# Optimization experiments

Hardware: AMD Instinct MI355X
Metric: run time of the kernel (lower is better)

## Reference

```python
import jax, jax.numpy as jnp
import numpy as np

CODEBOOK_SIZE = 8192
EMBED_DIM = 128
BETA = 0.25
TEMPERATURE = 0.1
EPS_NORM = 1e-12  # torch F.normalize eps


def _l2_normalize(x, axis=-1):
    n = jnp.linalg.norm(x, axis=axis, keepdims=True)
    return x / jnp.maximum(n, EPS_NORM)


def setup_inputs() -> dict:
    key = jax.random.key(0)
    kz, kw = jax.random.split(key)
    z = jax.random.normal(kz, (4, 4096, EMBED_DIM), dtype=jnp.float32)
    # torch init is uniform(-1/D, 1/D); normal also exercises the math fine,
    # but stay faithful to scale:
    W = jax.random.uniform(kw, (CODEBOOK_SIZE, EMBED_DIM), dtype=jnp.float32,
                           minval=-1.0 / EMBED_DIM, maxval=1.0 / EMBED_DIM)
    return {"z": z, "W": W}


def reference(z, W):
    orig_shape = z.shape
    z_flat = z.reshape(-1, EMBED_DIM)              # [N, D]
    N = z_flat.shape[0]

    z_norm = _l2_normalize(z_flat, axis=1)
    e_norm = _l2_normalize(W, axis=1)
    scores = z_norm @ e_norm.T                     # [N, K]

    idx = jnp.argmax(scores, axis=1)               # [N]
    z_q = W[idx].reshape(orig_shape)

    counts = jnp.zeros((CODEBOOK_SIZE,), jnp.float32).at[idx].add(1.0)
    e_mean = counts / N
    perplexity = jnp.exp(-jnp.sum(e_mean * jnp.log(e_mean + 1e-8)))

    sg = jax.lax.stop_gradient
    commit_loss = jnp.mean((sg(z_q) - z) ** 2) + BETA * jnp.mean((z_q - sg(z)) ** 2)

    z_q_st = z + sg(z_q - z)                        # straight-through

    log_probs = jax.nn.log_softmax(scores / TEMPERATURE, axis=1)  # [N, K]
    probs = jnp.exp(log_probs)
    P_avg = jnp.mean(probs, axis=0) + 1e-8
    entropy_loss = -jnp.sum(P_avg * jnp.log(P_avg))

    return (z_q_st, commit_loss, perplexity, entropy_loss)
```

## Files before the change

kernel.cpp:

```cpp
#include <hip/hip_runtime.h>
#include <hip/hip_bf16.h>
#include <math.h>

#define N_ROWS 16384
#define DIM 128
#define K_CODES 8192
#define EPS2 2e-3f
#define EPSF 7e-5f

#define OFF_EN       0u
#define OFF_ZN       1048576u
#define OFF_EP       3145728u
#define OFF_ZP       4194304u
#define OFF_ZC       6291456u
#define OFF_PART     7340032u
#define OFF_PART2    7602176u
#define OFF_LINV     7864320u
#define OFF_IDX      7880704u
#define OFF_FLA      7897088u
#define OFF_FLB      7913472u
#define OFF_CNT      7929856u
#define OFF_P        7938048u
#define OFF_MSE      7946240u
#define OFF_NFA      7946241u
#define OFF_NFB      7946242u
#define OFF_REFBUF   7946244u
#define MEMSET_BYTES 196624u

typedef __bf16 bf16x8 __attribute__((ext_vector_type(8)));
typedef float  f32x4  __attribute__((ext_vector_type(4)));
#define MFMA16(a, b, c) __builtin_amdgcn_mfma_f32_16x16x32_bf16(a, b, c, 0, 0, 0)

__device__ __forceinline__ void gld_lds16(const ushort* g, ushort* l) {
    __builtin_amdgcn_global_load_lds(
        (const __attribute__((address_space(1))) unsigned int*)g,
        (__attribute__((address_space(3))) unsigned int*)l, 16, 0, 0);
}

__device__ __forceinline__ ushort f2bf(float x) {
    __hip_bfloat16 b = __float2bfloat16(x);
    return *reinterpret_cast<ushort*>(&b);
}
__device__ __forceinline__ float bf2f(ushort u) {
    __hip_bfloat16 b = *reinterpret_cast<__hip_bfloat16*>(&u);
    return __bfloat162float(b);
}

__device__ __forceinline__ void bf_store2(ushort* __restrict__ P, int T, int r,
                                          int rx, int k, ushort e0, ushort e1) {
    int g = k >> 6, kp = (k >> 3) & 7, j = k & 7;
    int off = (((((T << 2) + g) << 10) + (r << 3) + (kp ^ rx)) << 3) + j;
    *reinterpret_cast<ushort2*>(&P[off]) = make_ushort2(e0, e1);
}

__global__ __launch_bounds__(256) void k_prep(const float* __restrict__ z,
                                              const float* __restrict__ W,
                                              float* __restrict__ zN,
                                              float* __restrict__ eN,
                                              ushort* __restrict__ Zp,
                                              ushort* __restrict__ Ep) {
    int t = threadIdx.x, w = t >> 6, lane = t & 63;
    int row = blockIdx.x * 4 + w;
    const float* src; float* dstN; ushort* dstP;
    if (row < N_ROWS) { src = z; dstN = zN; dstP = Zp; }
    else { row -= N_ROWS; src = W; dstN = eN; dstP = Ep; }
    float2 v = *reinterpret_cast<const float2*>(&src[(size_t)row * DIM + lane * 2]);
    float ss = v.x * v.x + v.y * v.y;
#pragma unroll
    for (int off = 32; off; off >>= 1) ss += __shfl_xor(ss, off);
    float nrm = fmaxf(sqrtf(ss), 1e-12f);
    float a = v.x / nrm, b = v.y / nrm;
    *reinterpret_cast<float2*>(&dstN[(size_t)row * DIM + lane * 2]) = make_float2(a, b);
    ushort ha = f2bf(a), hb = f2bf(b);
    ushort la = f2bf(a - bf2f(ha)), lb = f2bf(b - bf2f(hb));
    int T = row >> 7, r = row & 127, rx = r & 7, d = lane * 2;
    bf_store2(dstP, T, r, rx, d, ha, hb);
    bf_store2(dstP, T, r, rx, 128 + d, la, lb);
}

__global__ __launch_bounds__(256, 2) void k_p1(const ushort* __restrict__ Zp,
                                               const ushort* __restrict__ Ep,
                                               float4* __restrict__ part) {
    __shared__ ushort Bu[2][16384];
    int t = threadIdx.x, lane = t & 63, w = t >> 6;
    int rg = blockIdx.x >> 2, slice = blockIdx.x & 3;
    int wm = w >> 1, wn = w & 1;
    int n15 = lane & 15, quad = lane >> 4;
    int T = rg >> 1, rofs = (rg & 1) << 6;

    bf16x8 af[2][2][2];
#pragma unroll
    for (int ms = 0; ms < 2; ++ms) {
        int r = rofs + wm * 32 + ms * 16 + n15, rx = r & 7;
#pragma unroll
        for (int g = 0; g < 2; ++g)
#pragma unroll
            for (int kl = 0; kl < 2; ++kl)
                af[ms][g][kl] = *reinterpret_cast<const bf16x8*>(
                    &Zp[(((((T << 2) + g) << 10) + (r << 3) + (((kl * 4 + quad)) ^ rx)) << 3)]);
    }

    float sm[8], s2v[8], sl[8];
    unsigned si[8];
#pragma unroll
    for (int s = 0; s < 8; ++s) { sm[s] = -1e30f; s2v[s] = -1e30f; sl[s] = 0.f; si[s] = 0u; }

    {
        const ushort* gb = Ep + (((size_t)(slice * 16) << 2) << 13);
#pragma unroll
        for (int it = 0; it < 8; ++it) {
            int cpos = it * 256 + t;
            gld_lds16(gb + (cpos << 3), &Bu[0][cpos << 3]);
        }
    }
    int bufc = 0;
    for (int ch = 0; ch < 16; ++ch) {
        __syncthreads();
        if (ch < 15) {
            const ushort* gb = Ep + (((size_t)((slice * 16 + ch + 1) << 2)) << 13);
            ushort* dst = Bu[bufc ^ 1];
#pragma unroll
            for (int it = 0; it < 8; ++it) {
                int cpos = it * 256 + t;
                gld_lds16(gb + (cpos << 3), &dst[cpos << 3]);
            }
        }
        const ushort* bsrc = Bu[bufc];
        f32x4 acc[2][4];
#pragma unroll
        for (int i = 0; i < 2; ++i)
#pragma unroll
            for (int j = 0; j < 4; ++j) acc[i][j] = (f32x4)2.0f;
#pragma unroll
        for (int g = 0; g < 2; ++g)
#pragma unroll
            for (int kl = 0; kl < 2; ++kl) {
                bf16x8 bfr[4];
#pragma unroll
                for (int ns = 0; ns < 4; ++ns) {
                    int c = wn * 64 + ns * 16 + n15;
                    int kx = (kl * 4 + quad) ^ (c & 7);
                    bfr[ns] = *reinterpret_cast<const bf16x8*>(
                        &bsrc[(((g << 10) + (c << 3) + kx) << 3)]);
                }
#pragma unroll
                for (int ms = 0; ms < 2; ++ms)
#pragma unroll
                    for (int ns = 0; ns < 4; ++ns)
                        acc[ms][ns] = MFMA16(af[ms][g][kl], bfr[ns], acc[ms][ns]);
            }
        unsigned cbase = (unsigned)((slice * 16 + ch) * 128 + wn * 64 + n15);
#pragma unroll
        for (int ms = 0; ms < 2; ++ms)
#pragma unroll
            for (int reg = 0; reg < 4; ++reg) {
                int s = ms * 4 + reg;
                float m = sm[s], m2 = s2v[s], l = 0.f;
                unsigned idx = si[s];
#pragma unroll
                for (int ns = 0; ns < 4; ++ns) {
                    float v = acc[ms][ns][reg];
                    l += __expf(fmaf(v, 10.f, -20.f));
                    float lo = fminf(v, m);
                    m2 = fmaxf(m2, lo);
                    idx = (v > m) ? (cbase + ns * 16) : idx;
                    m = fmaxf(v, m);
                }
                sl[s] += l; sm[s] = m; s2v[s] = m2; si[s] = idx;
            }
        bufc ^= 1;
    }
#pragma unroll
    for (int ms = 0; ms < 2; ++ms)
#pragma unroll
        for (int reg = 0; reg < 4; ++reg) {
            int s = ms * 4 + reg;
            float m = sm[s], m2 = s2v[s], l = sl[s];
            unsigned idx = si[s];
#pragma unroll
            for (int off = 1; off < 16; off <<= 1) {
                float om  = __shfl_xor(m, off);
                float om2 = __shfl_xor(m2, off);
                float ol  = __shfl_xor(l, off);
                unsigned oi = (unsigned)__shfl_xor((int)idx, off);
                m2 = fmaxf(fmaxf(m2, om2), fminf(m, om));
                l += ol;
                bool take = (om > m) || (om == m && oi < idx);
                idx = take ? oi : idx;
                m = fmaxf(m, om);
            }
            if (n15 == 0) {
                int row = rg * 64 + wm * 32 + ms * 16 + quad * 4 + reg;
                part[slice * N_ROWS + row] = make_float4(m, l, __uint_as_float(idx), m2);
            }
        }
}

__global__ __launch_bounds__(256) void k_merge(const float4* __restrict__ part,
                                               float* __restrict__ linv_out,
                                               int* __restrict__ idx_out,
                                               unsigned int* __restrict__ counts,
                                               int* __restrict__ flaglistA,
                                               int* __restrict__ nfA) {
    int row = blockIdx.x * 256 + threadIdx.x;
    float m = -1e30f, m2 = -1e30f, l = 0.f;
    unsigned idx = 0u;
#pragma unroll
    for (int s = 0; s < 4; ++s) {
        float4 p = part[s * N_ROWS + row];
        float om = p.x, ol = p.y, om2 = p.w;
        unsigned oi = __float_as_uint(p.z);
        m2 = fmaxf(fmaxf(m2, om2), fminf(m, om));
        l += ol;
        bool take = (om > m) || (om == m && oi < idx);
        idx = take ? oi : idx;
        m = fmaxf(m, om);
    }
    linv_out[row] = 1.0f / l;
    idx_out[row] = (int)idx;
    atomicAdd(&counts[idx], 1u);
    if (m - m2 < EPS2) {
        int pos = atomicAdd(nfA, 1);
        if (pos < 8192) flaglistA[pos] = row;
    }
}

__global__ __launch_bounds__(256) void k_gather2(const ushort* __restrict__ Zp,
                                                 const int* __restrict__ flaglistA,
                                                 const int* __restrict__ nfA,
                                                 ushort* __restrict__ Zc) {
    int nf2 = *nfA; if (nf2 > 8192) nf2 = 8192;
    int total = nf2 * 32;
    const uint4* srcv = reinterpret_cast<const uint4*>(Zp);
    uint4* dstv = reinterpret_cast<uint4*>(Zc);
    for (int c = blockIdx.x * 256 + threadIdx.x; c < total; c += 65536) {
        int crow = c >> 5, g = (c >> 3) & 3, kp = c & 7;
        int row = flaglistA[crow];
        int Ts = row >> 7, rs = row & 127;
        int sidx = (((Ts << 2) + g) << 10) + (rs << 3) + (kp ^ (rs & 7));
        int Td = crow >> 6, rd = crow & 63;
        int didx = (((Td << 2) + g) << 9) + (rd << 3) + (kp ^ (rd & 7));
        dstv[didx] = srcv[sidx];
    }
}

__global__ __launch_bounds__(256, 2) void k_s2(const ushort* __restrict__ Zc,
                                               const ushort* __restrict__ Ep,
                                               const int* __restrict__ nfA,
                                               float4* __restrict__ part2) {
    __shared__ ushort Bu[2][8192];
    int nf2 = *nfA; if (nf2 > 8192) nf2 = 8192;
    int cg2 = blockIdx.x >> 3, csl = blockIdx.x & 7;
    if (cg2 * 64 >= nf2) return;
    int t = threadIdx.x, lane = t & 63, w = t >> 6;
    int wm = w >> 1, wn = w & 1;
    int n15 = lane & 15, quad = lane >> 4;

    bf16x8 af[2][4][2];
#pragma unroll
    for (int ms = 0; ms < 2; ++ms) {
        int r = wm * 32 + ms * 16 + n15, rx = r & 7;
#pragma unroll
        for (int gz = 0; gz < 4; ++gz)
#pragma unroll
            for (int kl = 0; kl < 2; ++kl)
                af[ms][gz][kl] = *reinterpret_cast<const bf16x8*>(
                    &Zc[(((((cg2 << 2) + gz) << 9) + (r << 3) + ((kl * 4 + quad) ^ rx)) << 3)]);
    }

    float sm[8], s2v[8];
    unsigned si[8];
#pragma unroll
    for (int s = 0; s < 8; ++s) { sm[s] = -1e30f; s2v[s] = -1e30f; si[s] = 0u; }

    {
        const ushort* gb = Ep + (((size_t)((csl * 8) << 2)) << 13);
#pragma unroll
        for (int it = 0; it < 4; ++it) {
            int cpos = it * 256 + t;
            gld_lds16(gb + (cpos << 3), &Bu[0][cpos << 3]);
        }
    }
    int bufc = 0;
    f32x4 acc[2][4];
#pragma unroll
    for (int i = 0; i < 2; ++i)
#pragma unroll
        for (int j = 0; j < 4; ++j) acc[i][j] = (f32x4)2.0f;

    for (int st = 0; st < 32; ++st) {
        __syncthreads();
        if (st < 31) {
            int nx = st + 1;
            const ushort* gb = Ep + (((size_t)(((csl * 8 + (nx >> 2)) << 2) + (nx & 3))) << 13);
            ushort* dst = Bu[bufc ^ 1];
#pragma unroll
            for (int it = 0; it < 4; ++it) {
                int cpos = it * 256 + t;
                gld_lds16(gb + (cpos << 3), &dst[cpos << 3]);
            }
        }
        const ushort* bsrc = Bu[bufc];
        int ge = st & 3;
        int a0 = ge & 1, a1 = (ge & 1) + 2;
        bool two = (ge < 2);
#pragma unroll
        for (int kl = 0; kl < 2; ++kl) {
            bf16x8 bfr[4];
#pragma unroll
            for (int ns = 0; ns < 4; ++ns) {
                int c = wn * 64 + ns * 16 + n15;
                int kx = (kl * 4 + quad) ^ (c & 7);
                bfr[ns] = *reinterpret_cast<const bf16x8*>(&bsrc[(((c << 3) + kx) << 3)]);
            }
#pragma unroll
            for (int ms = 0; ms < 2; ++ms)
#pragma unroll
                for (int ns = 0; ns < 4; ++ns)
                    acc[ms][ns] = MFMA16(af[ms][a0][kl], bfr[ns], acc[ms][ns]);
            if (two) {
#pragma unroll
                for (int ms = 0; ms < 2; ++ms)
#pragma unroll
                    for (int ns = 0; ns < 4; ++ns)
                        acc[ms][ns] = MFMA16(af[ms][a1][kl], bfr[ns], acc[ms][ns]);
            }
        }
        if (ge == 3) {
            int ch = st >> 2;
            unsigned cbase = (unsigned)((csl * 8 + ch) * 128 + wn * 64 + n15);
#pragma unroll
            for (int ms = 0; ms < 2; ++ms)
#pragma unroll
                for (int reg = 0; reg < 4; ++reg) {
                    int s = ms * 4 + reg;
                    float m = sm[s], m2 = s2v[s];
                    unsigned idx = si[s];
#pragma unroll
                    for (int ns = 0; ns < 4; ++ns) {
                        float v = acc[ms][ns][reg];
                        float lo = fminf(v, m);
                        m2 = fmaxf(m2, lo);
                        idx = (v > m) ? (cbase + ns * 16) : idx;
                        m = fmaxf(v, m);
                    }
                    sm[s] = m; s2v[s] = m2; si[s] = idx;
                }
#pragma unroll
            for (int i = 0; i < 2; ++i)
#pragma unroll
                for (int j = 0; j < 4; ++j) acc[i][j] = (f32x4)2.0f;
        }
        bufc ^= 1;
    }
#pragma unroll
    for (int ms = 0; ms < 2; ++ms)
#pragma unroll
        for (int reg = 0; reg < 4; ++reg) {
            int s = ms * 4 + reg;
            float m = sm[s], m2 = s2v[s];
            unsigned idx = si[s];
#pragma unroll
            for (int off = 1; off < 16; off <<= 1) {
                float om  = __shfl_xor(m, off);
                float om2 = __shfl_xor(m2, off);
                unsigned oi = (unsigned)__shfl_xor((int)idx, off);
                m2 = fmaxf(fmaxf(m2, om2), fminf(m, om));
                bool take = (om > m) || (om == m && oi < idx);
                idx = take ? oi : idx;
                m = fmaxf(m, om);
            }
            if (n15 == 0) {
                int crow = cg2 * 64 + wm * 32 + ms * 16 + quad * 4 + reg;
                part2[csl * 8192 + crow] = make_float4(m, 0.f, __uint_as_float(idx), m2);
            }
        }
}

__global__ __launch_bounds__(256) void k_merge2(const float4* __restrict__ part2,
                                                const int* __restrict__ flaglistA,
                                                const int* __restrict__ nfA,
                                                int* __restrict__ idx_arr,
                                                unsigned int* __restrict__ counts,
                                                int* __restrict__ flaglistB,
                                                int* __restrict__ nfB) {
    int i = blockIdx.x * 256 + threadIdx.x;
    int nf2 = *nfA; if (nf2 > 8192) nf2 = 8192;
    if (i >= nf2) return;
    int row = flaglistA[i];
    float m = -1e30f, m2 = -1e30f;
    unsigned idx = 0u;
#pragma unroll
    for (int s = 0; s < 8; ++s) {
        float4 p = part2[s * 8192 + i];
        float om = p.x, om2 = p.w;
        unsigned oi = __float_as_uint(p.z);
        m2 = fmaxf(fmaxf(m2, om2), fminf(m, om));
        bool take = (om > m) || (om == m && oi < idx);
        idx = take ? oi : idx;
        m = fmaxf(m, om);
    }
    int newi = (int)idx, oldi = idx_arr[row];
    if (newi != oldi) {
        idx_arr[row] = newi;
        atomicAdd(&counts[oldi], 0xFFFFFFFFu);
        atomicAdd(&counts[newi], 1u);
    }
    if (m - m2 < EPSF) {
        int pos = atomicAdd(nfB, 1);
        if (pos < N_ROWS) flaglistB[pos] = row;
    }
}

__global__ __launch_bounds__(256) void k_refine(const float* __restrict__ zN,
                                                const float* __restrict__ eN,
                                                const int* __restrict__ flaglistB,
                                                const int* __restrict__ nfB,
                                                unsigned long long* __restrict__ refbuf) {
    int nf = *nfB;
    if (nf > N_ROWS) nf = N_ROWS;
    int csl = blockIdx.x & 7;
    int t = threadIdx.x;
    __shared__ float zl[DIM];
    for (int fi = blockIdx.x >> 3; fi < nf; fi += 512) {
        int row = flaglistB[fi];
        __syncthreads();
        if (t < DIM) zl[t] = zN[(size_t)row * DIM + t];
        __syncthreads();
        double best = -1e300;
        int bc = 0x7FFFFFFF;
#pragma unroll
        for (int j = 0; j < 4; ++j) {
            int c = csl * 1024 + j * 256 + t;
            const float* e = &eN[(size_t)c * DIM];
            double s = 0.0;
#pragma unroll 8
            for (int d = 0; d < DIM; ++d) s += (double)zl[d] * (double)e[d];
            if (s > best) { best = s; bc = c; }
        }
#pragma unroll
        for (int off = 1; off < 64; off <<= 1) {
            double ob = __shfl_xor(best, off);
            int oc = __shfl_xor(bc, off);
            if (ob > best || (ob == best && oc < bc)) { best = ob; bc = oc; }
        }
        if ((t & 63) == 0) {
            unsigned long long u = (unsigned long long)__double_as_longlong(best);
            u = (u & 0x8000000000000000ull) ? ~u : (u | 0x8000000000000000ull);
            unsigned long long key = (u & ~0x1FFFull) | (unsigned long long)(8191 - bc);
            atomicMax(&refbuf[row], key);
        }
    }
}

__global__ __launch_bounds__(256) void k_fixidx(const int* __restrict__ flaglistB,
                                                const int* __restrict__ nfB,
                                                const unsigned long long* __restrict__ refbuf,
                                                int* __restrict__ idx,
                                                unsigned int* __restrict__ counts) {
    int i = blockIdx.x * 256 + threadIdx.x;
    int nf = *nfB;
    if (nf > N_ROWS) nf = N_ROWS;
    if (i < nf) {
        int row = flaglistB[i];
        int newi = 8191 - (int)(refbuf[row] & 0x1FFFull);
        int oldi = idx[row];
        if (newi != oldi) {
            idx[row] = newi;
            atomicAdd(&counts[oldi], 0xFFFFFFFFu);
            atomicAdd(&counts[newi], 1u);
        }
    }
}

__global__ __launch_bounds__(256, 2) void k_p2(const ushort* __restrict__ Zp,
                                               const ushort* __restrict__ Ep,
                                               const float* __restrict__ linv_in,
                                               float* __restrict__ P_sum) {
    __shared__ ushort Bu[2][16384];
    int t = threadIdx.x, lane = t & 63, w = t >> 6;
    int cg = blockIdx.x >> 2, rslice = blockIdx.x & 3;
    int wm = w >> 1, wn = w & 1;
    int n15 = lane & 15, quad = lane >> 4;
    int T = cg >> 1, cofs = (cg & 1) << 6;

    bf16x8 af[2][2][2];
#pragma unroll
    for (int ms = 0; ms < 2; ++ms) {
        int c = cofs + wm * 32 + ms * 16 + n15, cx = c & 7;
#pragma unroll
        for (int g = 0; g < 2; ++g)
#pragma unroll
            for (int kl = 0; kl < 2; ++kl)
                af[ms][g][kl] = *reinterpret_cast<const bf16x8*>(
                    &Ep[(((((T << 2) + g) << 10) + (c << 3) + ((kl * 4 + quad) ^ cx)) << 3)]);
    }

    float pacc[8];
#pragma unroll
    for (int s = 0; s < 8; ++s) pacc[s] = 0.f;

    {
        const ushort* gb = Zp + (((size_t)((rslice * 32) << 2)) << 13);
#pragma unroll
        for (int it = 0; it < 8; ++it) {
            int cpos = it * 256 + t;
            gld_lds16(gb + (cpos << 3), &Bu[0][cpos << 3]);
        }
    }
    int bufc = 0;
    for (int ch = 0; ch < 32; ++ch) {
        __syncthreads();
        if (ch < 31) {
            const ushort* gb = Zp + (((size_t)((rslice * 32 + ch + 1) << 2)) << 13);
            ushort* dst = Bu[bufc ^ 1];
#pragma unroll
            for (int it = 0; it < 8; ++it) {
                int cpos = it * 256 + t;
                gld_lds16(gb + (cpos << 3), &dst[cpos << 3]);
            }
        }
        const ushort* bsrc = Bu[bufc];
        f32x4 acc[2][4];
#pragma unroll
        for (int i = 0; i < 2; ++i)
#pragma unroll
            for (int j = 0; j < 4; ++j) acc[i][j] = (f32x4)2.0f;
#pragma unroll
        for (int g = 0; g < 2; ++g)
#pragma unroll
            for (int kl = 0; kl < 2; ++kl) {
                bf16x8 bfr[4];
#pragma unroll
                for (int ns = 0; ns < 4; ++ns) {
                    int r = wn * 64 + ns * 16 + n15;
                    int kx = (kl * 4 + quad) ^ (r & 7);
                    bfr[ns] = *reinterpret_cast<const bf16x8*>(
                        &bsrc[(((g << 10) + (r << 3) + kx) << 3)]);
                }
#pragma unroll
                for (int ms = 0; ms < 2; ++ms)
#pragma unroll
                    for (int ns = 0; ns < 4; ++ns)
                        acc[ms][ns] = MFMA16(af[ms][g][kl], bfr[ns], acc[ms][ns]);
            }
        int rbase = (rslice * 32 + ch) * 128 + wn * 64 + n15;
        float li[4];
#pragma unroll
        for (int ns = 0; ns < 4; ++ns) li[ns] = linv_in[rbase + ns * 16];
#pragma unroll
        for (int ms = 0; ms < 2; ++ms)
#pragma unroll
            for (int reg = 0; reg < 4; ++reg) {
                int s = ms * 4 + reg;
                float p = pacc[s];
#pragma unroll
                for (int ns = 0; ns < 4; ++ns)
                    p = fmaf(__expf(fmaf(acc[ms][ns][reg], 10.f, -20.f)), li[ns], p);
                pacc[s] = p;
            }
        bufc ^= 1;
    }
#pragma unroll
    for (int s = 0; s < 8; ++s) {
#pragma unroll
        for (int off = 1; off < 16; off <<= 1) pacc[s] += __shfl_xor(pacc[s], off);
    }
    if (n15 == 0) {
#pragma unroll
        for (int ms = 0; ms < 2; ++ms)
#pragma unroll
            for (int reg = 0; reg < 4; ++reg)
                atomicAdd(&P_sum[cg * 64 + wm * 32 + ms * 16 + quad * 4 + reg],
                          pacc[ms * 4 + reg]);
    }
}

__global__ __launch_bounds__(256) void k_gather(const float* __restrict__ z,
                                                const float* __restrict__ W,
                                                const int* __restrict__ idx,
                                                float* __restrict__ out,
                                                float* __restrict__ mse) {
    int v = blockIdx.x * 256 + threadIdx.x;
    int row = v >> 5;
    int id = idx[row];
    float4 q = *reinterpret_cast<const float4*>(&W[(size_t)id * DIM + (v & 31) * 4]);
    float4 zz = *reinterpret_cast<const float4*>(&z[(size_t)v * 4]);
    float dx = q.x - zz.x, dy = q.y - zz.y, dz = q.z - zz.z, dw = q.w - zz.w;
    *reinterpret_cast<float4*>(&out[(size_t)v * 4]) = q;
    float e = dx * dx + dy * dy + dz * dz + dw * dw;
#pragma unroll
    for (int off = 1; off < 64; off <<= 1) e += __shfl_xor(e, off);
    __shared__ float red[4];
    int lane = threadIdx.x & 63, wv = threadIdx.x >> 6;
    if (lane == 0) red[wv] = e;
    __syncthreads();
    if (threadIdx.x == 0) atomicAdd(mse, red[0] + red[1] + red[2] + red[3]);
}

__global__ __launch_bounds__(256) void k_finalize(const unsigned int* __restrict__ counts,
                                                  const float* __restrict__ P_sum,
                                                  const float* __restrict__ mse,
                                                  float* __restrict__ out) {
    int t = threadIdx.x;
    float s1 = 0.f, s2 = 0.f;
    for (int k = t; k < K_CODES; k += 256) {
        float em = (float)counts[k] * (1.0f / 16384.0f);
        s1 += em * logf(em + 1e-8f);
        float p = P_sum[k] * (1.0f / 16384.0f) + 1e-8f;
        s2 += p * logf(p);
    }
#pragma unroll
    for (int off = 1; off < 64; off <<= 1) {
        s1 += __shfl_xor(s1, off);
        s2 += __shfl_xor(s2, off);
    }
    __shared__ float r1[4], r2[4];
    int lane = t & 63, wv = t >> 6;
    if (lane == 0) { r1[wv] = s1; r2[wv] = s2; }
    __syncthreads();
    if (t == 0) {
        float S1 = r1[0] + r1[1] + r1[2] + r1[3];
        float S2 = r2[0] + r2[1] + r2[2] + r2[3];
        out[2097152] = 1.25f * mse[0] * (1.0f / 2097152.0f);
        out[2097153] = expf(-S1);
        out[2097154] = -S2;
    }
}

extern "C" void kernel_launch(void* const* d_in, const int* in_sizes, int n_in,
                              void* d_out, int out_size, void* d_ws, size_t ws_size,
                              hipStream_t stream) {
    (void)in_sizes; (void)n_in; (void)out_size; (void)ws_size;
    const float* z = (const float*)d_in[0];
    const float* W = (const float*)d_in[1];
    float* ws = (float*)d_ws;
    float* eN = ws + OFF_EN;
    float* zN = ws + OFF_ZN;
    ushort* Ep = (ushort*)(ws + OFF_EP);
    ushort* Zp = (ushort*)(ws + OFF_ZP);
    ushort* Zc = (ushort*)(ws + OFF_ZC);
    float4* part = (float4*)(ws + OFF_PART);
    float4* part2 = (float4*)(ws + OFF_PART2);
    float* linv = ws + OFF_LINV;
    int* idx = (int*)(ws + OFF_IDX);
    int* flaglistA = (int*)(ws + OFF_FLA);
    int* flaglistB = (int*)(ws + OFF_FLB);
    unsigned int* counts = (unsigned int*)(ws + OFF_CNT);
    float* P = ws + OFF_P;
    float* mse = ws + OFF_MSE;
    int* nfA = (int*)(ws + OFF_NFA);
    int* nfB = (int*)(ws + OFF_NFB);
    unsigned long long* refbuf = (unsigned long long*)(ws + OFF_REFBUF);
    float* out = (float*)d_out;

    hipMemsetAsync(ws + OFF_CNT, 0, MEMSET_BYTES, stream);
    k_prep<<<(N_ROWS + K_CODES) / 4, 256, 0, stream>>>(z, W, zN, eN, Zp, Ep);
    k_p1<<<1024, 256, 0, stream>>>(Zp, Ep, part);
    k_merge<<<N_ROWS / 256, 256, 0, stream>>>(part, linv, idx, counts, flaglistA, nfA);
    k_gather2<<<256, 256, 0, stream>>>(Zp, flaglistA, nfA, Zc);
    k_s2<<<1024, 256, 0, stream>>>(Zc, Ep, nfA, part2);
    k_merge2<<<32, 256, 0, stream>>>(part2, flaglistA, nfA, idx, counts, flaglistB, nfB);
    k_refine<<<4096, 256, 0, stream>>>(zN, eN, flaglistB, nfB, refbuf);
    k_fixidx<<<64, 256, 0, stream>>>(flaglistB, nfB, refbuf, idx, counts);
    k_p2<<<512, 256, 0, stream>>>(Zp, Ep, linv, P);
    k_gather<<<(N_ROWS * DIM / 4) / 256, 256, 0, stream>>>(z, W, idx, out, mse);
    k_finalize<<<1, 256, 0, stream>>>(counts, P, mse, out);
}
```

Before: 306.0 us.

## Prescale z by temperature·log2e, use exp2, halve LDS tiles for higher occupancy

Folds the 1/temperature scale and log2(e) into the normalized z operand during prep, so the softmax exponent becomes a bare exp2 of the MFMA output, with the accumulator initialised to 2.0 as the shift. The argmax/second-max thresholds are rescaled to match. The pass-1 and pass-2 GEMM kernels now use 64-column LDS chunks instead of 128, halving shared memory and accumulator registers and raising launch bounds from 2 to 4 blocks per CU, at the cost of twice as many chunk iterations and barriers. The second-max update is replaced with a single med3 instruction.

```diff
diff --git a/kernel.cpp b/kernel.cpp
--- a/kernel.cpp
+++ b/kernel.cpp
@@ -5,8 +5,9 @@
 #define N_ROWS 16384
 #define DIM 128
 #define K_CODES 8192
-#define EPS2 2e-3f
-#define EPSF 7e-5f
+#define SCALE_LOG2E 14.4269504088896341f
+#define EPS2 0.0288539f
+#define EPSF 1.00989e-3f
 
 #define OFF_EN       0u
 #define OFF_ZN       1048576u
@@ -31,6 +32,15 @@
 typedef float  f32x4  __attribute__((ext_vector_type(4)));
 #define MFMA16(a, b, c) __builtin_amdgcn_mfma_f32_16x16x32_bf16(a, b, c, 0, 0, 0)
 
+#if defined(__has_builtin)
+#if __has_builtin(__builtin_amdgcn_exp2f)
+#define EXP2(x) __builtin_amdgcn_exp2f(x)
+#endif
+#endif
+#ifndef EXP2
+#define EXP2(x) __expf(0.69314718055994531f * (x))
+#endif
+
 __device__ __forceinline__ void gld_lds16(const ushort* g, ushort* l) {
     __builtin_amdgcn_global_load_lds(
         (const __attribute__((address_space(1))) unsigned int*)g,
@@ -61,9 +71,9 @@
                                               ushort* __restrict__ Ep) {
     int t = threadIdx.x, w = t >> 6, lane = t & 63;
     int row = blockIdx.x * 4 + w;
-    const float* src; float* dstN; ushort* dstP;
-    if (row < N_ROWS) { src = z; dstN = zN; dstP = Zp; }
-    else { row -= N_ROWS; src = W; dstN = eN; dstP = Ep; }
+    const float* src; float* dstN; ushort* dstP; float sc;
+    if (row < N_ROWS) { src = z; dstN = zN; dstP = Zp; sc = SCALE_LOG2E; }
+    else { row -= N_ROWS; src = W; dstN = eN; dstP = Ep; sc = 1.0f; }
     float2 v = *reinterpret_cast<const float2*>(&src[(size_t)row * DIM + lane * 2]);
     float ss = v.x * v.x + v.y * v.y;
 #pragma unroll
@@ -71,17 +81,18 @@
     float nrm = fmaxf(sqrtf(ss), 1e-12f);
     float a = v.x / nrm, b = v.y / nrm;
     *reinterpret_cast<float2*>(&dstN[(size_t)row * DIM + lane * 2]) = make_float2(a, b);
-    ushort ha = f2bf(a), hb = f2bf(b);
-    ushort la = f2bf(a - bf2f(ha)), lb = f2bf(b - bf2f(hb));
+    float as = a * sc, bs = b * sc;
+    ushort ha = f2bf(as), hb = f2bf(bs);
+    ushort la = f2bf(as - bf2f(ha)), lb = f2bf(bs - bf2f(hb));
     int T = row >> 7, r = row & 127, rx = r & 7, d = lane * 2;
     bf_store2(dstP, T, r, rx, d, ha, hb);
     bf_store2(dstP, T, r, rx, 128 + d, la, lb);
 }
 
-__global__ __launch_bounds__(256, 2) void k_p1(const ushort* __restrict__ Zp,
+__global__ __launch_bounds__(256, 4) void k_p1(const ushort* __restrict__ Zp,
                                                const ushort* __restrict__ Ep,
                                                float4* __restrict__ part) {
-    __shared__ ushort Bu[2][16384];
+    __shared__ ushort Bu[2][8192];
     int t = threadIdx.x, lane = t & 63, w = t >> 6;
     int rg = blockIdx.x >> 2, slice = blockIdx.x & 3;
     int wm = w >> 1, wn = w & 1;
@@ -106,67 +117,71 @@
     for (int s = 0; s < 8; ++s) { sm[s] = -1e30f; s2v[s] = -1e30f; sl[s] = 0.f; si[s] = 0u; }
 
     {
-        const ushort* gb = Ep + (((size_t)(slice * 16) << 2) << 13);
-#pragma unroll
-        for (int it = 0; it < 8; ++it) {
+        int Te = slice * 16, re = 0;
+#pragma unroll
+        for (int it = 0; it < 4; ++it) {
             int cpos = it * 256 + t;
-            gld_lds16(gb + (cpos << 3), &Bu[0][cpos << 3]);
+            int g = cpos >> 9, loc = cpos & 511;
+            gld_lds16(Ep + ((((Te << 2) + g) << 13) + (re << 6) + (loc << 3)),
+                      &Bu[0][cpos << 3]);
         }
     }
     int bufc = 0;
-    for (int ch = 0; ch < 16; ++ch) {
+    for (int ch = 0; ch < 32; ++ch) {
         __syncthreads();
-        if (ch < 15) {
-            const ushort* gb = Ep + (((size_t)((slice * 16 + ch + 1) << 2)) << 13);
+        if (ch < 31) {
+            int nx = ch + 1;
+            int Te = slice * 16 + (nx >> 1), re = (nx & 1) << 6;
             ushort* dst = Bu[bufc ^ 1];
 #pragma unroll
-            for (int it = 0; it < 8; ++it) {
+            for (int it = 0; it < 4; ++it) {
                 int cpos = it * 256 + t;
-                gld_lds16(gb + (cpos << 3), &dst[cpos << 3]);
+                int g = cpos >> 9, loc = cpos & 511;
+                gld_lds16(Ep + ((((Te << 2) + g) << 13) + (re << 6) + (loc << 3)),
+                          &dst[cpos << 3]);
             }
         }
         const ushort* bsrc = Bu[bufc];
-        f32x4 acc[2][4];
+        f32x4 acc[2][2];
 #pragma unroll
         for (int i = 0; i < 2; ++i)
 #pragma unroll
-            for (int j = 0; j < 4; ++j) acc[i][j] = (f32x4)2.0f;
+            for (int j = 0; j < 2; ++j) acc[i][j] = (f32x4)2.0f;
 #pragma unroll
         for (int g = 0; g < 2; ++g)
 #pragma unroll
             for (int kl = 0; kl < 2; ++kl) {
-                bf16x8 bfr[4];
-#pragma unroll
-                for (int ns = 0; ns < 4; ++ns) {
-                    int c = wn * 64 + ns * 16 + n15;
+                bf16x8 bfr[2];
+#pragma unroll
+                for (int ns = 0; ns < 2; ++ns) {
+                    int c = wn * 32 + ns * 16 + n15;
                     int kx = (kl * 4 + quad) ^ (c & 7);
                     bfr[ns] = *reinterpret_cast<const bf16x8*>(
-                        &bsrc[(((g << 10) + (c << 3) + kx) << 3)]);
+                        &bsrc[(((g << 9) + (c << 3) + kx) << 3)]);
                 }
 #pragma unroll
                 for (int ms = 0; ms < 2; ++ms)
 #pragma unroll
-                    for (int ns = 0; ns < 4; ++ns)
+                    for (int ns = 0; ns < 2; ++ns)
                         acc[ms][ns] = MFMA16(af[ms][g][kl], bfr[ns], acc[ms][ns]);
             }
-        unsigned cbase = (unsigned)((slice * 16 + ch) * 128 + wn * 64 + n15);
+        unsigned cbase = (unsigned)(slice * 2048 + ch * 64 + wn * 32 + n15);
 #pragma unroll
         for (int ms = 0; ms < 2; ++ms)
 #pragma unroll
             for (int reg = 0; reg < 4; ++reg) {
                 int s = ms * 4 + reg;
-                float m = sm[s], m2 = s2v[s], l = 0.f;
+                float m = sm[s], m2 = s2v[s], l = sl[s];
                 unsigned idx = si[s];
 #pragma unroll
-                for (int ns = 0; ns < 4; ++ns) {
+                for (int ns = 0; ns < 2; ++ns) {
                     float v = acc[ms][ns][reg];
-                    l += __expf(fmaf(v, 10.f, -20.f));
-                    float lo = fminf(v, m);
-                    m2 = fmaxf(m2, lo);
+                    l += EXP2(v);
+                    m2 = __builtin_amdgcn_fmed3f(v, m, m2);
                     idx = (v > m) ? (cbase + ns * 16) : idx;
                     m = fmaxf(v, m);
                 }
-                sl[s] += l; sm[s] = m; s2v[s] = m2; si[s] = idx;
+                sl[s] = l; sm[s] = m; s2v[s] = m2; si[s] = idx;
             }
         bufc ^= 1;
     }
@@ -339,8 +354,7 @@
 #pragma unroll
                     for (int ns = 0; ns < 4; ++ns) {
                         float v = acc[ms][ns][reg];
-                        float lo = fminf(v, m);
-                        m2 = fmaxf(m2, lo);
+                        m2 = __builtin_amdgcn_fmed3f(v, m, m2);
                         idx = (v > m) ? (cbase + ns * 16) : idx;
                         m = fmaxf(v, m);
                     }
@@ -473,11 +487,11 @@
     }
 }
 
-__global__ __launch_bounds__(256, 2) void k_p2(const ushort* __restrict__ Zp,
+__global__ __launch_bounds__(256, 4) void k_p2(const ushort* __restrict__ Zp,
                                                const ushort* __restrict__ Ep,
                                                const float* __restrict__ linv_in,
                                                float* __restrict__ P_sum) {
-    __shared__ ushort Bu[2][16384];
+    __shared__ ushort Bu[2][8192];
     int t = threadIdx.x, lane = t & 63, w = t >> 6;
     int cg = blockIdx.x >> 2, rslice = blockIdx.x & 3;
     int wm = w >> 1, wn = w & 1;
@@ -501,53 +515,58 @@
     for (int s = 0; s < 8; ++s) pacc[s] = 0.f;
 
     {
-        const ushort* gb = Zp + (((size_t)((rslice * 32) << 2)) << 13);
-#pragma unroll
-        for (int it = 0; it < 8; ++it) {
+        int Tz = rslice * 32, re = 0;
+#pragma unroll
+        for (int it = 0; it < 4; ++it) {
             int cpos = it * 256 + t;
-            gld_lds16(gb + (cpos << 3), &Bu[0][cpos << 3]);
+            int g = cpos >> 9, loc = cpos & 511;
+            gld_lds16(Zp + ((((Tz << 2) + g) << 13) + (re << 6) + (loc << 3)),
+                      &Bu[0][cpos << 3]);
         }
     }
     int bufc = 0;
-    for (int ch = 0; ch < 32; ++ch) {
+    for (int ch = 0; ch < 64; ++ch) {
         __syncthreads();
-        if (ch < 31) {
-            const ushort* gb = Zp + (((size_t)((rslice * 32 + ch + 1) << 2)) << 13);
+        if (ch < 63) {
+            int nx = ch + 1;
+            int Tz = rslice * 32 + (nx >> 1), re = (nx & 1) << 6;
             ushort* dst = Bu[bufc ^ 1];
 #pragma unroll
-            for (int it = 0; it < 8; ++it) {
+            for (int it = 0; it < 4; ++it) {
                 int cpos = it * 256 + t;
-                gld_lds16(gb + (cpos << 3), &dst[cpos << 3]);
+                int g = cpos >> 9, loc = cpos & 511;
+                gld_lds16(Zp + ((((Tz << 2) + g) << 13) + (re << 6) + (loc << 3)),
+                          &dst[cpos << 3]);
             }
         }
         const ushort* bsrc = Bu[bufc];
-        f32x4 acc[2][4];
+        f32x4 acc[2][2];
 #pragma unroll
         for (int i = 0; i < 2; ++i)
 #pragma unroll
-            for (int j = 0; j < 4; ++j) acc[i][j] = (f32x4)2.0f;
+            for (int j = 0; j < 2; ++j) acc[i][j] = (f32x4)2.0f;
 #pragma unroll
         for (int g = 0; g < 2; ++g)
 #pragma unroll
             for (int kl = 0; kl < 2; ++kl) {
-                bf16x8 bfr[4];
-#pragma unroll
-                for (int ns = 0; ns < 4; ++ns) {
-                    int r = wn * 64 + ns * 16 + n15;
+                bf16x8 bfr[2];
+#pragma unroll
+                for (int ns = 0; ns < 2; ++ns) {
+                    int r = wn * 32 + ns * 16 + n15;
                     int kx = (kl * 4 + quad) ^ (r & 7);
                     bfr[ns] = *reinterpret_cast<const bf16x8*>(
-                        &bsrc[(((g << 10) + (r << 3) + kx) << 3)]);
+                        &bsrc[(((g << 9) + (r << 3) + kx) << 3)]);
                 }
 #pragma unroll
                 for (int ms = 0; ms < 2; ++ms)
 #pragma unroll
-                    for (int ns = 0; ns < 4; ++ns)
+                    for (int ns = 0; ns < 2; ++ns)
                         acc[ms][ns] = MFMA16(af[ms][g][kl], bfr[ns], acc[ms][ns]);
             }
-        int rbase = (rslice * 32 + ch) * 128 + wn * 64 + n15;
-        float li[4];
-#pragma unroll
-        for (int ns = 0; ns < 4; ++ns) li[ns] = linv_in[rbase + ns * 16];
+        int rbase = rslice * 4096 + ch * 64 + wn * 32 + n15;
+        float li[2];
+#pragma unroll
+        for (int ns = 0; ns < 2; ++ns) li[ns] = linv_in[rbase + ns * 16];
 #pragma unroll
         for (int ms = 0; ms < 2; ++ms)
 #pragma unroll
@@ -555,8 +574,8 @@
                 int s = ms * 4 + reg;
                 float p = pacc[s];
 #pragma unroll
-                for (int ns = 0; ns < 4; ++ns)
-                    p = fmaf(__expf(fmaf(acc[ms][ns][reg], 10.f, -20.f)), li[ns], p);
+                for (int ns = 0; ns < 2; ++ns)
+                    p = fmaf(EXP2(acc[ms][ns][reg]), li[ns], p);
                 pacc[s] = p;
             }
         bufc ^= 1;
```

New measurement: 299.0 us, median of 2. 2.3% less time.
